# Kernel tuning notes

Hardware: AMD Instinct MI355X
Metric: run time of the kernel (lower is better)

The kernel has to match this reference:

```python
import jax, jax.numpy as jnp
import numpy as np

NPOINT = 1024
RADIUS = 0.2
NSAMPLE = 64
BN_EPS = 1e-5


def setup_inputs() -> dict:
    key = jax.random.key(0)
    ks = jax.random.split(key, 16)
    B, N = 8, 8192
    inp = {
        "xyz": jax.random.normal(ks[0], (B, 3, N), jnp.float32),
        "points": jax.random.normal(ks[1], (B, 3, N), jnp.float32),
        "seed_inds": jax.random.randint(ks[2], (B, N), 0, N),
    }
    chans = [6, 64, 64, 128]
    for i in range(3):
        cin, cout = chans[i], chans[i + 1]
        kk = jax.random.split(ks[3 + i], 3)
        inp[f"w{i}"] = jax.random.normal(kk[0], (cout, cin), jnp.float32) / np.sqrt(cin)
        inp[f"b{i}"] = jnp.zeros((cout,), jnp.float32)
        inp[f"g{i}"] = jnp.ones((cout,), jnp.float32)
        inp[f"be{i}"] = jnp.zeros((cout,), jnp.float32)
        inp[f"m{i}"] = jax.random.normal(kk[1], (cout,), jnp.float32) * 0.1
        inp[f"v{i}"] = jax.random.uniform(kk[2], (cout,), jnp.float32, 0.5, 1.5)
    return inp


def _fps(xyz, npoint):
    # xyz: [B, N, 3]. Deterministic start at index 0 (torch uses a random start).
    B, N, _ = xyz.shape

    def step(carry, _):
        dist, far = carry
        cent = jnp.take_along_axis(xyz, far[:, None, None], axis=1)  # [B,1,3]
        d = jnp.sum((xyz - cent) ** 2, -1)                           # [B,N]
        dist = jnp.minimum(dist, d)
        nxt = jnp.argmax(dist, -1)
        return (dist, nxt), far

    init = (jnp.full((B, N), 1e10, xyz.dtype), jnp.zeros((B,), jnp.int32))
    _, idxs = jax.lax.scan(step, init, None, length=npoint)
    return idxs.T  # [B, npoint]


def _sqdist(src, dst):
    # src [B,S,3], dst [B,N,3] -> [B,S,N]
    d = -2.0 * jnp.einsum("bsc,bnc->bsn", src, dst)
    d += jnp.sum(src ** 2, -1)[:, :, None]
    d += jnp.sum(dst ** 2, -1)[:, None, :]
    return d


def _gather(pts, idx):
    # pts [B,N,C], idx [B,S,K] -> [B,S,K,C]
    B, S, K = idx.shape
    flat = jnp.take_along_axis(pts, idx.reshape(B, S * K, 1), axis=1)
    return flat.reshape(B, S, K, pts.shape[-1])


def _forward(xyz, points, seed_inds, layers):
    xyz_t = xyz.transpose(0, 2, 1)      # [B,N,3]
    pts_t = points.transpose(0, 2, 1)   # [B,N,D]
    B, N, _ = xyz_t.shape

    fps_idx = _fps(xyz_t, NPOINT)                                   # [B,S]
    new_seed = jnp.take_along_axis(seed_inds, fps_idx.astype(seed_inds.dtype), axis=1)
    new_xyz = jnp.take_along_axis(xyz_t, fps_idx[:, :, None], axis=1)  # [B,S,3]

    # ball query via sort trick (same math as torch module)
    sq = _sqdist(new_xyz, xyz_t)                                    # [B,S,N]
    gi = jnp.where(sq > RADIUS ** 2, N, jnp.arange(N, dtype=jnp.int32)[None, None, :])
    gi = jnp.sort(gi, axis=-1)[:, :, :NSAMPLE]                      # [B,S,K]
    first = gi[:, :, :1]
    gi = jnp.where(gi == N, first, gi)

    gxyz = _gather(xyz_t, gi) - new_xyz[:, :, None, :]              # [B,S,K,3]
    gpts = _gather(pts_t, gi)                                       # [B,S,K,D]
    feat = jnp.concatenate([gxyz, gpts], -1)                        # [B,S,K,3+D]

    for (w, b, g, be, m, v) in layers:
        feat = jnp.einsum("bskc,oc->bsko", feat, w) + b             # 1x1 conv
        feat = (feat - m) * (g / jnp.sqrt(v + BN_EPS)) + be         # BN (inference)
        feat = jax.nn.relu(feat)

    new_points = jnp.max(feat, axis=2).transpose(0, 2, 1)           # [B,Cout,S]
    return new_xyz.transpose(0, 2, 1), new_points, new_seed


def reference(xyz, points, seed_inds,
              w0, b0, g0, be0, m0, v0,
              w1, b1, g1, be1, m1, v1,
              w2, b2, g2, be2, m2, v2):
    layers = [(w0, b0, g0, be0, m0, v0),
              (w1, b1, g1, be1, m1, v1),
              (w2, b2, g2, be2, m2, v2)]
    return _forward(xyz, points, seed_inds, layers)
```

## Files before the change

### kernel.cpp

```cpp
#include <hip/hip_runtime.h>

#define B_ 8
#define N_ 8192
#define S_ 1024
#define NS_ 64

typedef float v2f __attribute__((ext_vector_type(2)));
typedef unsigned long long u64;
typedef short bf16x8 __attribute__((ext_vector_type(8)));
typedef float f32x4 __attribute__((ext_vector_type(4)));

#define OUT0 0
#define OUT1 24576
#define OUT2 1073152

template <int CTRL>
static __device__ __forceinline__ float dpp_max_step(float v) {
    int o = __builtin_amdgcn_update_dpp(__float_as_int(v), __float_as_int(v),
                                        CTRL, 0xf, 0xf, false);
    return fmaxf(v, __int_as_float(o));
}
static __device__ __forceinline__ float wave_max_f32(float v) {
    v = dpp_max_step<0x111>(v);
    v = dpp_max_step<0x112>(v);
    v = dpp_max_step<0x114>(v);
    v = dpp_max_step<0x118>(v);
    v = dpp_max_step<0x142>(v);
    v = dpp_max_step<0x143>(v);
    return __int_as_float(__builtin_amdgcn_readlane(__float_as_int(v), 63));
}
template <int CTRL>
static __device__ __forceinline__ unsigned dpp_umin_step(unsigned v) {
    unsigned o = (unsigned)__builtin_amdgcn_update_dpp((int)v, (int)v,
                                                       CTRL, 0xf, 0xf, false);
    return v < o ? v : o;
}
static __device__ __forceinline__ unsigned wave_min_u32(unsigned v) {
    v = dpp_umin_step<0x111>(v);
    v = dpp_umin_step<0x112>(v);
    v = dpp_umin_step<0x114>(v);
    v = dpp_umin_step<0x118>(v);
    v = dpp_umin_step<0x142>(v);
    v = dpp_umin_step<0x143>(v);
    return (unsigned)__builtin_amdgcn_readlane((int)v, 63);
}

static __device__ __forceinline__ short f2bf(float f) {
    unsigned u = __float_as_uint(f);
    return (short)((u + 0x7FFFu + ((u >> 16) & 1u)) >> 16);
}

#define FPS_T 256
#define FPS_J 16

__global__ __launch_bounds__(FPS_T, 1) void fps_kernel(const float* __restrict__ xyz,
                                                       float* out) {
    const int b = blockIdx.x;
    const int t = threadIdx.x;
    const int lane = t & 63;
    const int wq = t >> 6;
    const float* X = xyz + b * 3 * N_;

    __shared__ float4 xyzq[N_];
    __shared__ u64 slots[8];
    __shared__ float seedL[S_];

    v2f px2[FPS_J], py2[FPS_J], pz2[FPS_J], dist2[FPS_J];
#pragma unroll
    for (int j = 0; j < FPS_J; ++j) {
        int n = t + 512 * j;
        float x0 = X[n],          x1 = X[n + 256];
        float y0 = X[N_ + n],     y1 = X[N_ + n + 256];
        float z0 = X[2 * N_ + n], z1 = X[2 * N_ + n + 256];
        px2[j] = (v2f){x0, x1};
        py2[j] = (v2f){y0, y1};
        pz2[j] = (v2f){z0, z1};
        dist2[j] = (v2f){1e10f, 1e10f};
        xyzq[n]       = make_float4(x0, y0, z0, 0.f);
        xyzq[n + 256] = make_float4(x1, y1, z1, 0.f);
    }
    __syncthreads();

    int ci = 0;
    float c0 = X[0], c1 = X[N_], c2 = X[2 * N_];

    for (int step = 0; step < S_; ++step) {
        if (t == 0) seedL[step] = __int_as_float(ci);

        v2f mv = (v2f){-1.0f, -1.0f};
        {
#pragma clang fp contract(off)
            v2f c0v = (v2f){c0, c0};
            v2f c1v = (v2f){c1, c1};
            v2f c2v = (v2f){c2, c2};
#pragma unroll
            for (int j = 0; j < FPS_J; ++j) {
                v2f e0 = px2[j] - c0v;
                v2f e1 = py2[j] - c1v;
                v2f e2 = pz2[j] - c2v;
                v2f q0 = e0 * e0;
                v2f q1 = e1 * e1;
                v2f q2 = e2 * e2;
                v2f d  = (q0 + q1) + q2;
                v2f dm = __builtin_elementwise_min(dist2[j], d);
                dist2[j] = dm;
                mv = __builtin_elementwise_max(mv, dm);
            }
        }
        float m = fmaxf(mv.x, mv.y);

        unsigned mask = 0u;
#pragma unroll
        for (int j = 0; j < FPS_J; ++j) {
            if (dist2[j].x == m) mask |= (1u << (2 * j));
            if (dist2[j].y == m) mask |= (1u << (2 * j + 1));
        }
        float wmax = wave_max_f32(m);

        unsigned c = (unsigned)(__ffs(mask) - 1);
        unsigned cand = (m == wmax) ? ((unsigned)t | (c << 8)) : 0xffffffffu;
        unsigned widx = wave_min_u32(cand);

        if (lane == 63) {
            u64 key = ((u64)__float_as_uint(wmax) << 13) | (u64)(8191u - widx);
            slots[((step & 1) << 2) + wq] = key;
        }
        __syncthreads();

        const u64* sp = &slots[(step & 1) << 2];
        u64 k0 = sp[0], k1 = sp[1], k2 = sp[2], k3 = sp[3];
        int i0 = 8191 - (int)(k0 & 0x1fffull);
        int i1 = 8191 - (int)(k1 & 0x1fffull);
        int i2 = 8191 - (int)(k2 & 0x1fffull);
        int i3 = 8191 - (int)(k3 & 0x1fffull);
        float4 p0 = xyzq[i0];
        float4 p1 = xyzq[i1];
        float4 p2 = xyzq[i2];
        float4 p3 = xyzq[i3];
        bool b01 = k0 > k1, b23 = k2 > k3;
        u64 ka = b01 ? k0 : k1;
        u64 kb = b23 ? k2 : k3;
        float4 pa, pb;
        pa.x = b01 ? p0.x : p1.x; pa.y = b01 ? p0.y : p1.y; pa.z = b01 ? p0.z : p1.z;
        pb.x = b23 ? p2.x : p3.x; pb.y = b23 ? p2.y : p3.y; pb.z = b23 ? p2.z : p3.z;
        bool bab = ka > kb;
        u64 km = bab ? ka : kb;
        ci = 8191 - (int)(km & 0x1fffull);
        c0 = bab ? pa.x : pb.x;
        c1 = bab ? pa.y : pb.y;
        c2 = bab ? pa.z : pb.z;
    }

    __syncthreads();
    float* oseed = out + OUT2 + b * S_;
#pragma unroll
    for (int k = 0; k < 4; ++k)
        oseed[t + 256 * k] = seedL[t + 256 * k];
}

__global__ __launch_bounds__(256) void wconv_kernel(const float* __restrict__ w1,
                                                    const float* __restrict__ w2,
                                                    short* __restrict__ wbf) {
    int t = blockIdx.x * 256 + threadIdx.x;
    float v = (t < 4096) ? w1[t] : w2[t - 4096];
    wbf[t] = f2bf(v);
}

__global__ __launch_bounds__(256) void down_kernel(
    const float* __restrict__ xyz, const float* __restrict__ pts,
    const int* __restrict__ seed,
    const float* __restrict__ w0, const float* __restrict__ b0,
    const float* __restrict__ g0, const float* __restrict__ be0,
    const float* __restrict__ m0, const float* __restrict__ v0,
    const float* __restrict__ w1, const float* __restrict__ b1,
    const float* __restrict__ g1, const float* __restrict__ be1,
    const float* __restrict__ m1, const float* __restrict__ v1,
    const float* __restrict__ w2, const float* __restrict__ b2,
    const float* __restrict__ g2, const float* __restrict__ be2,
    const float* __restrict__ m2, const float* __restrict__ v2,
    float* out, const short* __restrict__ wbf) {
    const int sg = blockIdx.x;
    const int b = sg >> 9, sp = sg & 511;
    const int s0 = sp << 1;
    const int t = threadIdx.x;
    const int lane = t & 63;
    const int wq = __builtin_amdgcn_readfirstlane(t >> 6);
    const int ln = lane & 15;
    const int quad = (lane >> 4) & 3;

    __shared__ float f0[2][64 * 9];
    __shared__ short feat[2][64 * 72];
    __shared__ float wmaxs[2][4 * 132];
    __shared__ float scs[256], ofs[256];
    __shared__ int cand[2][4 * 64];
    __shared__ int cnts[2][4];
    __shared__ int gis[2][64];

    const float* X = xyz + b * 3 * N_;

    int ci0 = __float_as_int(out[OUT2 + b * S_ + s0]) & 8191;
    int ci1 = __float_as_int(out[OUT2 + b * S_ + s0 + 1]) & 8191;
    float cx0 = X[ci0], cy0 = X[N_ + ci0], cz0 = X[2 * N_ + ci0];
    float cx1 = X[ci1], cy1 = X[N_ + ci1], cz1 = X[2 * N_ + ci1];

    {
        float sc, of;
        if (t < 64) {
            int c = t;
            sc = g0[c] / sqrtf(v0[c] + 1e-5f);
            of = (b0[c] - m0[c]) * sc + be0[c];
        } else if (t < 128) {
            int c = t - 64;
            sc = g1[c] / sqrtf(v1[c] + 1e-5f);
            of = (b1[c] - m1[c]) * sc + be1[c];
        } else {
            int c = t - 128;
            sc = g2[c] / sqrtf(v2[c] + 1e-5f);
            of = (b2[c] - m2[c]) * sc + be2[c];
        }
        scs[t] = sc;
        ofs[t] = of;
    }
    __syncthreads();

    if (t < 2) {
        int cc = t;
        int ci = cc ? ci1 : ci0;
        out[OUT0 + (b * 3 + 0) * S_ + s0 + cc] = cc ? cx1 : cx0;
        out[OUT0 + (b * 3 + 1) * S_ + s0 + cc] = cc ? cy1 : cy0;
        out[OUT0 + (b * 3 + 2) * S_ + s0 + cc] = cc ? cz1 : cz0;
        out[OUT2 + b * S_ + s0 + cc] = (float)seed[b * N_ + ci];
    }

    {
        int cnt0 = 0, cnt1 = 0;
        const int wbase = wq << 11;
#pragma unroll 2
        for (int base = 0; base < 2048; base += 128) {
            int n0 = wbase + base + lane;
            int n1 = n0 + 64;
            float x0 = X[n0], y0 = X[N_ + n0], z0 = X[2 * N_ + n0];
            float x1 = X[n1], y1 = X[N_ + n1], z1 = X[2 * N_ + n1];

            float e0 = x0 - cx0, e1 = y0 - cy0, e2 = z0 - cz0;
            float dA0 = fmaf(e2, e2, fmaf(e1, e1, e0 * e0));
            float f0_ = x0 - cx1, f1_ = y0 - cy1, f2_ = z0 - cz1;
            float dB0 = fmaf(f2_, f2_, fmaf(f1_, f1_, f0_ * f0_));
            float q0 = x1 - cx0, q1 = y1 - cy0, q2 = z1 - cz0;
            float dA1 = fmaf(q2, q2, fmaf(q1, q1, q0 * q0));
            float r0 = x1 - cx1, r1 = y1 - cy1, r2 = z1 - cz1;
            float dB1 = fmaf(r2, r2, fmaf(r1, r1, r0 * r0));

            u64 mA0 = __ballot(dA0 <= 0.04f);
            if (mA0) {
                int pos = cnt0 + (int)__popcll(mA0 & ((1ull << lane) - 1ull));
                if ((dA0 <= 0.04f) && pos < NS_) cand[0][(wq << 6) + pos] = n0;
                cnt0 += (int)__popcll(mA0);
            }
            u64 mB0 = __ballot(dB0 <= 0.04f);
            if (mB0) {
                int pos = cnt1 + (int)__popcll(mB0 & ((1ull << lane) - 1ull));
                if ((dB0 <= 0.04f) && pos < NS_) cand[1][(wq << 6) + pos] = n0;
                cnt1 += (int)__popcll(mB0);
            }
            u64 mA1 = __ballot(dA1 <= 0.04f);
            if (mA1) {
                int pos = cnt0 + (int)__popcll(mA1 & ((1ull << lane) - 1ull));
                if ((dA1 <= 0.04f) && pos < NS_) cand[0][(wq << 6) + pos] = n1;
                cnt0 += (int)__popcll(mA1);
            }
            u64 mB1 = __ballot(dB1 <= 0.04f);
            if (mB1) {
                int pos = cnt1 + (int)__popcll(mB1 & ((1ull << lane) - 1ull));
                if ((dB1 <= 0.04f) && pos < NS_) cand[1][(wq << 6) + pos] = n1;
                cnt1 += (int)__popcll(mB1);
            }
        }
        if (lane == 0) { cnts[0][wq] = cnt0; cnts[1][wq] = cnt1; }
    }
    __syncthreads();

    if (t < 128) {
        int cc = t >> 6, k = t & 63;
        int start = 0, sel = -1, firstv = -1;
#pragma unroll
        for (int w = 0; w < 4; ++w) {
            int cw = min(cnts[cc][w], NS_);
            if (firstv < 0 && cw > 0) firstv = cand[cc][(w << 6)];
            if (sel < 0 && k < start + cw) sel = cand[cc][(w << 6) + (k - start)];
            start += cw;
        }
        if (sel < 0) sel = firstv;
        gis[cc][k] = sel;
    }
    __syncthreads();

    if (t < 128) {
        int cc = t >> 6, k = t & 63;
        int gidx = gis[cc][k] & 8191;
        const float* P = pts + b * 3 * N_;
        float ccx = cc ? cx1 : cx0;
        float ccy = cc ? cy1 : cy0;
        float ccz = cc ? cz1 : cz0;
        f0[cc][k * 9 + 0] = X[gidx] - ccx;
        f0[cc][k * 9 + 1] = X[N_ + gidx] - ccy;
        f0[cc][k * 9 + 2] = X[2 * N_ + gidx] - ccz;
        f0[cc][k * 9 + 3] = P[gidx];
        f0[cc][k * 9 + 4] = P[N_ + gidx];
        f0[cc][k * 9 + 5] = P[2 * N_ + gidx];
    }
    __syncthreads();

#pragma unroll 1
    for (int cc = 0; cc < 2; ++cc) {
        float in[6];
#pragma unroll
        for (int c = 0; c < 6; ++c) in[c] = f0[cc][lane * 9 + c];
#pragma unroll 1
        for (int i = 0; i < 16; i += 4) {
            int o = wq * 16 + i;
            float a0 = 0.f, a1 = 0.f, a2 = 0.f, a3 = 0.f;
#pragma unroll
            for (int c = 0; c < 6; ++c) {
                float rc = in[c];
                a0 = fmaf(rc, w0[(o + 0) * 6 + c], a0);
                a1 = fmaf(rc, w0[(o + 1) * 6 + c], a1);
                a2 = fmaf(rc, w0[(o + 2) * 6 + c], a2);
                a3 = fmaf(rc, w0[(o + 3) * 6 + c], a3);
            }
            feat[cc][lane * 72 + o + 0] = f2bf(fmaxf(fmaf(a0, scs[o + 0], ofs[o + 0]), 0.f));
            feat[cc][lane * 72 + o + 1] = f2bf(fmaxf(fmaf(a1, scs[o + 1], ofs[o + 1]), 0.f));
            feat[cc][lane * 72 + o + 2] = f2bf(fmaxf(fmaf(a2, scs[o + 2], ofs[o + 2]), 0.f));
            feat[cc][lane * 72 + o + 3] = f2bf(fmaxf(fmaf(a3, scs[o + 3], ofs[o + 3]), 0.f));
        }
    }
    __syncthreads();

    const int arow = 16 * wq + ln;
    const bool usebf = (wbf != nullptr);

    {
        bf16x8 a1f[2][2];
#pragma unroll
        for (int cc = 0; cc < 2; ++cc)
#pragma unroll
            for (int ks = 0; ks < 2; ++ks)
                a1f[cc][ks] = *(const bf16x8*)&feat[cc][arow * 72 + ks * 32 + quad * 8];

#pragma unroll
        for (int nt = 0; nt < 4; ++nt) {
            f32x4 acc0 = {0.f, 0.f, 0.f, 0.f};
            f32x4 acc1 = {0.f, 0.f, 0.f, 0.f};
#pragma unroll
            for (int ks = 0; ks < 2; ++ks) {
                int off = (nt * 16 + ln) * 64 + ks * 32 + quad * 8;
                bf16x8 bf;
                if (usebf) {
                    bf = *(const bf16x8*)&wbf[off];
                } else {
                    const float* wr = w1 + off;
                    float4 p = *(const float4*)wr;
                    float4 q = *(const float4*)(wr + 4);
                    bf = (bf16x8){f2bf(p.x), f2bf(p.y), f2bf(p.z), f2bf(p.w),
                                  f2bf(q.x), f2bf(q.y), f2bf(q.z), f2bf(q.w)};
                }
                acc0 = __builtin_amdgcn_mfma_f32_16x16x32_bf16(a1f[0][ks], bf, acc0, 0, 0, 0);
                acc1 = __builtin_amdgcn_mfma_f32_16x16x32_bf16(a1f[1][ks], bf, acc1, 0, 0, 0);
            }
            int o = nt * 16 + ln;
            float sc = scs[64 + o], of = ofs[64 + o];
#pragma unroll
            for (int reg = 0; reg < 4; ++reg) {
                float y0 = fmaxf(fmaf(acc0[reg], sc, of), 0.f);
                float y1 = fmaxf(fmaf(acc1[reg], sc, of), 0.f);
                feat[0][(16 * wq + quad * 4 + reg) * 72 + o] = f2bf(y0);
                feat[1][(16 * wq + quad * 4 + reg) * 72 + o] = f2bf(y1);
            }
        }
    }

    {
        bf16x8 a2f[2][2];
#pragma unroll
        for (int cc = 0; cc < 2; ++cc)
#pragma unroll
            for (int ks = 0; ks < 2; ++ks)
                a2f[cc][ks] = *(const bf16x8*)&feat[cc][arow * 72 + ks * 32 + quad * 8];

#pragma unroll
        for (int nt = 0; nt < 8; ++nt) {
            f32x4 acc0 = {0.f, 0.f, 0.f, 0.f};
            f32x4 acc1 = {0.f, 0.f, 0.f, 0.f};
#pragma unroll
            for (int ks = 0; ks < 2; ++ks) {
                int off = (nt * 16 + ln) * 64 + ks * 32 + quad * 8;
                bf16x8 bf;
                if (usebf) {
                    bf = *(const bf16x8*)&wbf[4096 + off];
                } else {
                    const float* wr = w2 + off;
                    float4 p = *(const float4*)wr;
                    float4 q = *(const float4*)(wr + 4);
                    bf = (bf16x8){f2bf(p.x), f2bf(p.y), f2bf(p.z), f2bf(p.w),
                                  f2bf(q.x), f2bf(q.y), f2bf(q.z), f2bf(q.w)};
                }
                acc0 = __builtin_amdgcn_mfma_f32_16x16x32_bf16(a2f[0][ks], bf, acc0, 0, 0, 0);
                acc1 = __builtin_amdgcn_mfma_f32_16x16x32_bf16(a2f[1][ks], bf, acc1, 0, 0, 0);
            }
            int o = nt * 16 + ln;
            float sc = scs[128 + o], of = ofs[128 + o];
            float m0_ = -1.f, m1_ = -1.f;
#pragma unroll
            for (int reg = 0; reg < 4; ++reg) {
                m0_ = fmaxf(m0_, fmaxf(fmaf(acc0[reg], sc, of), 0.f));
                m1_ = fmaxf(m1_, fmaxf(fmaf(acc1[reg], sc, of), 0.f));
            }
            m0_ = fmaxf(m0_, __shfl_xor(m0_, 16, 64));
            m0_ = fmaxf(m0_, __shfl_xor(m0_, 32, 64));
            m1_ = fmaxf(m1_, __shfl_xor(m1_, 16, 64));
            m1_ = fmaxf(m1_, __shfl_xor(m1_, 32, 64));
            if (lane < 16) {
                wmaxs[0][wq * 132 + o] = m0_;
                wmaxs[1][wq * 132 + o] = m1_;
            }
        }
    }
    __syncthreads();

    {
        int cc = t >> 7, ch = t & 127;
        float m = fmaxf(fmaxf(wmaxs[cc][0 * 132 + ch], wmaxs[cc][1 * 132 + ch]),
                        fmaxf(wmaxs[cc][2 * 132 + ch], wmaxs[cc][3 * 132 + ch]));
        out[OUT1 + (b * 128 + ch) * S_ + s0 + cc] = m;
    }
}

extern "C" void kernel_launch(void* const* d_in, const int* in_sizes, int n_in,
                              void* d_out, int out_size, void* d_ws, size_t ws_size,
                              hipStream_t stream) {
    const float* xyz  = (const float*)d_in[0];
    const float* pts  = (const float*)d_in[1];
    const int*   seed = (const int*)d_in[2];
    const float* w0 = (const float*)d_in[3];
    const float* b0 = (const float*)d_in[4];
    const float* g0 = (const float*)d_in[5];
    const float* be0 = (const float*)d_in[6];
    const float* m0 = (const float*)d_in[7];
    const float* v0 = (const float*)d_in[8];
    const float* w1 = (const float*)d_in[9];
    const float* b1 = (const float*)d_in[10];
    const float* g1 = (const float*)d_in[11];
    const float* be1 = (const float*)d_in[12];
    const float* m1 = (const float*)d_in[13];
    const float* v1 = (const float*)d_in[14];
    const float* w2 = (const float*)d_in[15];
    const float* b2 = (const float*)d_in[16];
    const float* g2 = (const float*)d_in[17];
    const float* be2 = (const float*)d_in[18];
    const float* m2 = (const float*)d_in[19];
    const float* v2 = (const float*)d_in[20];
    float* out = (float*)d_out;

    short* wbf = nullptr;
    if (ws_size >= 12288 * sizeof(short)) {
        wbf = (short*)d_ws;
        wconv_kernel<<<dim3(48), dim3(256), 0, stream>>>(w1, w2, wbf);
    }

    fps_kernel<<<dim3(B_), dim3(FPS_T), 0, stream>>>(xyz, out);
    down_kernel<<<dim3(B_ * S_ / 2), dim3(256), 0, stream>>>(xyz, pts, seed,
        w0, b0, g0, be0, m0, v0,
        w1, b1, g1, be1, m1, v1,
        w2, b2, g2, be2, m2, v2,
        out, wbf);
}
```

Baseline: 1.168 ms.

## Use 8 waves per down_kernel block, one wave group per center

Doubles down_kernel's block size to 512 threads. The ball-query scan is split across 8 waves of 1024 points each, and candidate merging now walks 8 per-wave lists. In the MLP stages each group of four waves handles one of the two centers, instead of every wave looping over both. This shortens each wave's serial work and register footprint, at the cost of larger blocks with more shared memory for candidates and possibly lower block-level occupancy. The FPS kernel, which is likely the dominant cost, is unchanged.

```diff
diff --git a/kernel.cpp b/kernel.cpp
--- a/kernel.cpp
+++ b/kernel.cpp
@@ -166,7 +166,7 @@
     wbf[t] = f2bf(v);
 }
 
-__global__ __launch_bounds__(256) void down_kernel(
+__global__ __launch_bounds__(512) void down_kernel(
     const float* __restrict__ xyz, const float* __restrict__ pts,
     const int* __restrict__ seed,
     const float* __restrict__ w0, const float* __restrict__ b0,
@@ -184,7 +184,9 @@
     const int s0 = sp << 1;
     const int t = threadIdx.x;
     const int lane = t & 63;
-    const int wq = __builtin_amdgcn_readfirstlane(t >> 6);
+    const int w8 = __builtin_amdgcn_readfirstlane(t >> 6);
+    const int wq = w8 & 3;
+    const int wcc = w8 >> 2;
     const int ln = lane & 15;
     const int quad = (lane >> 4) & 3;
 
@@ -192,8 +194,8 @@
     __shared__ short feat[2][64 * 72];
     __shared__ float wmaxs[2][4 * 132];
     __shared__ float scs[256], ofs[256];
-    __shared__ int cand[2][4 * 64];
-    __shared__ int cnts[2][4];
+    __shared__ int cand[2][8 * 64];
+    __shared__ int cnts[2][8];
     __shared__ int gis[2][64];
 
     const float* X = xyz + b * 3 * N_;
@@ -203,7 +205,7 @@
     float cx0 = X[ci0], cy0 = X[N_ + ci0], cz0 = X[2 * N_ + ci0];
     float cx1 = X[ci1], cy1 = X[N_ + ci1], cz1 = X[2 * N_ + ci1];
 
-    {
+    if (t < 192) {
         float sc, of;
         if (t < 64) {
             int c = t;
@@ -234,9 +236,9 @@
 
     {
         int cnt0 = 0, cnt1 = 0;
-        const int wbase = wq << 11;
+        const int wbase = w8 << 10;
 #pragma unroll 2
-        for (int base = 0; base < 2048; base += 128) {
+        for (int base = 0; base < 1024; base += 128) {
             int n0 = wbase + base + lane;
             int n1 = n0 + 64;
             float x0 = X[n0], y0 = X[N_ + n0], z0 = X[2 * N_ + n0];
@@ -254,29 +256,29 @@
             u64 mA0 = __ballot(dA0 <= 0.04f);
             if (mA0) {
                 int pos = cnt0 + (int)__popcll(mA0 & ((1ull << lane) - 1ull));
-                if ((dA0 <= 0.04f) && pos < NS_) cand[0][(wq << 6) + pos] = n0;
+                if ((dA0 <= 0.04f) && pos < NS_) cand[0][(w8 << 6) + pos] = n0;
                 cnt0 += (int)__popcll(mA0);
             }
             u64 mB0 = __ballot(dB0 <= 0.04f);
             if (mB0) {
                 int pos = cnt1 + (int)__popcll(mB0 & ((1ull << lane) - 1ull));
-                if ((dB0 <= 0.04f) && pos < NS_) cand[1][(wq << 6) + pos] = n0;
+                if ((dB0 <= 0.04f) && pos < NS_) cand[1][(w8 << 6) + pos] = n0;
                 cnt1 += (int)__popcll(mB0);
             }
             u64 mA1 = __ballot(dA1 <= 0.04f);
             if (mA1) {
                 int pos = cnt0 + (int)__popcll(mA1 & ((1ull << lane) - 1ull));
-                if ((dA1 <= 0.04f) && pos < NS_) cand[0][(wq << 6) + pos] = n1;
+                if ((dA1 <= 0.04f) && pos < NS_) cand[0][(w8 << 6) + pos] = n1;
                 cnt0 += (int)__popcll(mA1);
             }
             u64 mB1 = __ballot(dB1 <= 0.04f);
             if (mB1) {
                 int pos = cnt1 + (int)__popcll(mB1 & ((1ull << lane) - 1ull));
-                if ((dB1 <= 0.04f) && pos < NS_) cand[1][(wq << 6) + pos] = n1;
+                if ((dB1 <= 0.04f) && pos < NS_) cand[1][(w8 << 6) + pos] = n1;
                 cnt1 += (int)__popcll(mB1);
             }
         }
-        if (lane == 0) { cnts[0][wq] = cnt0; cnts[1][wq] = cnt1; }
+        if (lane == 0) { cnts[0][w8] = cnt0; cnts[1][w8] = cnt1; }
     }
     __syncthreads();
 
@@ -284,7 +286,7 @@
         int cc = t >> 6, k = t & 63;
         int start = 0, sel = -1, firstv = -1;
 #pragma unroll
-        for (int w = 0; w < 4; ++w) {
+        for (int w = 0; w < 8; ++w) {
             int cw = min(cnts[cc][w], NS_);
             if (firstv < 0 && cw > 0) firstv = cand[cc][(w << 6)];
             if (sel < 0 && k < start + cw) sel = cand[cc][(w << 6) + (k - start)];
@@ -311,11 +313,10 @@
     }
     __syncthreads();
 
-#pragma unroll 1
-    for (int cc = 0; cc < 2; ++cc) {
+    {
         float in[6];
 #pragma unroll
-        for (int c = 0; c < 6; ++c) in[c] = f0[cc][lane * 9 + c];
+        for (int c = 0; c < 6; ++c) in[c] = f0[wcc][lane * 9 + c];
 #pragma unroll 1
         for (int i = 0; i < 16; i += 4) {
             int o = wq * 16 + i;
@@ -328,10 +329,10 @@
                 a2 = fmaf(rc, w0[(o + 2) * 6 + c], a2);
                 a3 = fmaf(rc, w0[(o + 3) * 6 + c], a3);
             }
-            feat[cc][lane * 72 + o + 0] = f2bf(fmaxf(fmaf(a0, scs[o + 0], ofs[o + 0]), 0.f));
-            feat[cc][lane * 72 + o + 1] = f2bf(fmaxf(fmaf(a1, scs[o + 1], ofs[o + 1]), 0.f));
-            feat[cc][lane * 72 + o + 2] = f2bf(fmaxf(fmaf(a2, scs[o + 2], ofs[o + 2]), 0.f));
-            feat[cc][lane * 72 + o + 3] = f2bf(fmaxf(fmaf(a3, scs[o + 3], ofs[o + 3]), 0.f));
+            feat[wcc][lane * 72 + o + 0] = f2bf(fmaxf(fmaf(a0, scs[o + 0], ofs[o + 0]), 0.f));
+            feat[wcc][lane * 72 + o + 1] = f2bf(fmaxf(fmaf(a1, scs[o + 1], ofs[o + 1]), 0.f));
+            feat[wcc][lane * 72 + o + 2] = f2bf(fmaxf(fmaf(a2, scs[o + 2], ofs[o + 2]), 0.f));
+            feat[wcc][lane * 72 + o + 3] = f2bf(fmaxf(fmaf(a3, scs[o + 3], ofs[o + 3]), 0.f));
         }
     }
     __syncthreads();
@@ -340,17 +341,14 @@
     const bool usebf = (wbf != nullptr);
 
     {
-        bf16x8 a1f[2][2];
-#pragma unroll
-        for (int cc = 0; cc < 2; ++cc)
-#pragma unroll
-            for (int ks = 0; ks < 2; ++ks)
-                a1f[cc][ks] = *(const bf16x8*)&feat[cc][arow * 72 + ks * 32 + quad * 8];
+        bf16x8 a1f[2];
+#pragma unroll
+        for (int ks = 0; ks < 2; ++ks)
+            a1f[ks] = *(const bf16x8*)&feat[wcc][arow * 72 + ks * 32 + quad * 8];
 
 #pragma unroll
         for (int nt = 0; nt < 4; ++nt) {
-            f32x4 acc0 = {0.f, 0.f, 0.f, 0.f};
-            f32x4 acc1 = {0.f, 0.f, 0.f, 0.f};
+            f32x4 acc = {0.f, 0.f, 0.f, 0.f};
 #pragma unroll
             for (int ks = 0; ks < 2; ++ks) {
                 int off = (nt * 16 + ln) * 64 + ks * 32 + quad * 8;
@@ -364,33 +362,27 @@
                     bf = (bf16x8){f2bf(p.x), f2bf(p.y), f2bf(p.z), f2bf(p.w),
                                   f2bf(q.x), f2bf(q.y), f2bf(q.z), f2bf(q.w)};
                 }
-                acc0 = __builtin_amdgcn_mfma_f32_16x16x32_bf16(a1f[0][ks], bf, acc0, 0, 0, 0);
-                acc1 = __builtin_amdgcn_mfma_f32_16x16x32_bf16(a1f[1][ks], bf, acc1, 0, 0, 0);
+                acc = __builtin_amdgcn_mfma_f32_16x16x32_bf16(a1f[ks], bf, acc, 0, 0, 0);
             }
             int o = nt * 16 + ln;
             float sc = scs[64 + o], of = ofs[64 + o];
 #pragma unroll
             for (int reg = 0; reg < 4; ++reg) {
-                float y0 = fmaxf(fmaf(acc0[reg], sc, of), 0.f);
-                float y1 = fmaxf(fmaf(acc1[reg], sc, of), 0.f);
-                feat[0][(16 * wq + quad * 4 + reg) * 72 + o] = f2bf(y0);
-                feat[1][(16 * wq + quad * 4 + reg) * 72 + o] = f2bf(y1);
+                float y = fmaxf(fmaf(acc[reg], sc, of), 0.f);
+                feat[wcc][(16 * wq + quad * 4 + reg) * 72 + o] = f2bf(y);
             }
         }
     }
 
     {
-        bf16x8 a2f[2][2];
-#pragma unroll
-        for (int cc = 0; cc < 2; ++cc)
-#pragma unroll
-            for (int ks = 0; ks < 2; ++ks)
-                a2f[cc][ks] = *(const bf16x8*)&feat[cc][arow * 72 + ks * 32 + quad * 8];
+        bf16x8 a2f[2];
+#pragma unroll
+        for (int ks = 0; ks < 2; ++ks)
+            a2f[ks] = *(const bf16x8*)&feat[wcc][arow * 72 + ks * 32 + quad * 8];
 
 #pragma unroll
         for (int nt = 0; nt < 8; ++nt) {
-            f32x4 acc0 = {0.f, 0.f, 0.f, 0.f};
-            f32x4 acc1 = {0.f, 0.f, 0.f, 0.f};
+            f32x4 acc = {0.f, 0.f, 0.f, 0.f};
 #pragma unroll
             for (int ks = 0; ks < 2; ++ks) {
                 int off = (nt * 16 + ln) * 64 + ks * 32 + quad * 8;
@@ -404,30 +396,24 @@
                     bf = (bf16x8){f2bf(p.x), f2bf(p.y), f2bf(p.z), f2bf(p.w),
                                   f2bf(q.x), f2bf(q.y), f2bf(q.z), f2bf(q.w)};
                 }
-                acc0 = __builtin_amdgcn_mfma_f32_16x16x32_bf16(a2f[0][ks], bf, acc0, 0, 0, 0);
-                acc1 = __builtin_amdgcn_mfma_f32_16x16x32_bf16(a2f[1][ks], bf, acc1, 0, 0, 0);
+                acc = __builtin_amdgcn_mfma_f32_16x16x32_bf16(a2f[ks], bf, acc, 0, 0, 0);
             }
             int o = nt * 16 + ln;
             float sc = scs[128 + o], of = ofs[128 + o];
-            float m0_ = -1.f, m1_ = -1.f;
+            float m = -1.f;
 #pragma unroll
             for (int reg = 0; reg < 4; ++reg) {
-                m0_ = fmaxf(m0_, fmaxf(fmaf(acc0[reg], sc, of), 0.f));
-                m1_ = fmaxf(m1_, fmaxf(fmaf(acc1[reg], sc, of), 0.f));
-            }
-            m0_ = fmaxf(m0_, __shfl_xor(m0_, 16, 64));
-            m0_ = fmaxf(m0_, __shfl_xor(m0_, 32, 64));
-            m1_ = fmaxf(m1_, __shfl_xor(m1_, 16, 64));
-            m1_ = fmaxf(m1_, __shfl_xor(m1_, 32, 64));
-            if (lane < 16) {
-                wmaxs[0][wq * 132 + o] = m0_;
-                wmaxs[1][wq * 132 + o] = m1_;
-            }
-        }
-    }
-    __syncthreads();
-
-    {
+                float y = fmaxf(fmaf(acc[reg], sc, of), 0.f);
+                m = fmaxf(m, y);
+            }
+            m = fmaxf(m, __shfl_xor(m, 16, 64));
+            m = fmaxf(m, __shfl_xor(m, 32, 64));
+            if (lane < 16) wmaxs[wcc][wq * 132 + o] = m;
+        }
+    }
+    __syncthreads();
+
+    if (t < 256) {
         int cc = t >> 7, ch = t & 127;
         float m = fmaxf(fmaxf(wmaxs[cc][0 * 132 + ch], wmaxs[cc][1 * 132 + ch]),
                         fmaxf(wmaxs[cc][2 * 132 + ch], wmaxs[cc][3 * 132 + ch]));
@@ -468,7 +454,7 @@
     }
 
     fps_kernel<<<dim3(B_), dim3(FPS_T), 0, stream>>>(xyz, out);
-    down_kernel<<<dim3(B_ * S_ / 2), dim3(256), 0, stream>>>(xyz, pts, seed,
+    down_kernel<<<dim3(B_ * S_ / 2), dim3(512), 0, stream>>>(xyz, pts, seed,
         w0, b0, g0, be0, m0, v0,
         w1, b1, g1, be1, m1, v1,
         w2, b2, g2, be2, m2, v2,
```

New measurement: 1.205 ms. 1.03x slower.
